# Kernel tuning notes

Hardware: AMD Instinct MI355X
Metric: run time of the kernel (lower is better)

Reference implementation:

```python
import jax, jax.numpy as jnp
import numpy as np

B, S, D, E = 4, 4096, 1024, 8

def setup_inputs() -> dict:
    key = jax.random.key(0)
    k1, k2, k3, k4, k5 = jax.random.split(key, 5)
    scale = 1.0 / np.sqrt(D)
    return {
        "x": jax.random.normal(k1, (B, S, D), dtype=jnp.float32),
        "Wg": jax.random.normal(k2, (D, D), dtype=jnp.float32) * scale,   # gate Linear(D, D)
        "bg": jnp.zeros((D,), dtype=jnp.float32),
        "We": jax.random.normal(k3, (E, D, D), dtype=jnp.float32) * scale,  # per-expert Linear(D, D)
        "be": jnp.zeros((E, D), dtype=jnp.float32),
    }

def reference(x, Wg, bg, We, be):
    # gating network: Linear + Softmax over last dim (size D, per the original module)
    probs = jax.nn.softmax(x @ Wg + bg, axis=-1)           # [B,S,D]
    idx = jnp.argmax(probs, axis=-1)                        # [B,S], values in [0, D)
    p = jnp.take_along_axis(probs, idx[..., None], axis=-1)[..., 0]  # top-1 gate prob
    e_idx = idx % We.shape[0]                               # map argmax to expert id
    # run every expert densely, then select routed expert per token (top-1 switch routing)
    h = jax.nn.relu(jnp.einsum('bsd,edf->besf', x, We) + be[None, :, None, :])  # [B,E,S,D]
    onehot = jax.nn.one_hot(e_idx, We.shape[0], dtype=x.dtype)                   # [B,S,E]
    out = jnp.einsum('besf,bse->bsf', h, onehot) * p[..., None]                  # [B,S,D]
    return out
```

## Files before the change

kernel.cpp:

```cpp
#include <hip/hip_runtime.h>
#include <stdint.h>
#include <stddef.h>

#define TOK    16384
#define DDIM   1024
#define NEXP   8
#define BMT    128
#define RB_MAX 136
#define MARGIN 2.5e-2f
#define AMBIG_CAP 4096
#define BK     64

typedef __bf16 bf16x8 __attribute__((ext_vector_type(8)));
typedef float  f32x4  __attribute__((ext_vector_type(4)));
typedef unsigned short u16x8 __attribute__((ext_vector_type(8)));

__device__ __forceinline__ unsigned short f2bf(float f) {
    unsigned int u = __float_as_uint(f);
    u += 0x7fff + ((u >> 16) & 1);
    return (unsigned short)(u >> 16);
}

__device__ __forceinline__ void gload_lds16(const void* g, void* l) {
    __builtin_amdgcn_global_load_lds(
        (const __attribute__((address_space(1))) unsigned int*)g,
        (__attribute__((address_space(3))) unsigned int*)l, 16, 0, 0);
}

__global__ __launch_bounds__(256) void cvt_x(
    const float* __restrict__ x, unsigned short* __restrict__ xbf)
{
    const size_t t = ((size_t)blockIdx.x * 256 + threadIdx.x) * 8;
    const float4 v0 = *(const float4*)(x + t);
    const float4 v1 = *(const float4*)(x + t + 4);
    const float vv[8] = {v0.x, v0.y, v0.z, v0.w, v1.x, v1.y, v1.z, v1.w};
    u16x8 hh;
#pragma unroll
    for (int j = 0; j < 8; j++) hh[j] = f2bf(vv[j]);
    *(u16x8*)(xbf + t) = hh;
}

__global__ __launch_bounds__(256) void transpose_mat(
    const float* __restrict__ src0, unsigned short* __restrict__ dst0)
{
    __shared__ float tile[32][33];
    const int e  = blockIdx.z;
    const int k0 = blockIdx.x * 32;
    const int n0 = blockIdx.y * 32;
    const int tx = threadIdx.x;
    const int ty = threadIdx.y;
    const float* src = src0 + (size_t)e * DDIM * DDIM;
    unsigned short* dst = dst0 + (size_t)e * DDIM * DDIM;
#pragma unroll
    for (int r = 0; r < 4; r++)
        tile[ty + r * 8][tx] = src[(size_t)(k0 + ty + r * 8) * DDIM + n0 + tx];
    __syncthreads();
#pragma unroll
    for (int r = 0; r < 4; r++)
        dst[(size_t)(n0 + ty + r * 8) * DDIM + k0 + tx] = f2bf(tile[tx][ty + r * 8]);
}

__global__ __launch_bounds__(256) void gating_mfma(
    const unsigned short* __restrict__ xbf,
    const unsigned short* __restrict__ WgT,
    const float* __restrict__ bg, float* __restrict__ logits)
{
    __shared__ unsigned short Asm[128 * BK];
    __shared__ unsigned short Bsm[128 * BK];
    const int rb = blockIdx.x;
    const int nb = blockIdx.y;
    const int tid  = threadIdx.x;
    const int lane = tid & 63;
    const int wave = tid >> 6;
    const int q    = lane >> 4;
    const int m16  = lane & 15;
    const int wrow = (wave & 1) * 64;
    const int wcol = (wave >> 1) * 64;

    const unsigned short* Ag = xbf + (size_t)rb * 128 * DDIM;
    const unsigned short* Bg = WgT + (size_t)nb * 128 * DDIM;

    const unsigned short* pa[4];
    const unsigned short* pb[4];
#pragma unroll
    for (int i = 0; i < 4; i++) {
        const int idx = tid + i * 256;
        const int r = idx >> 3;
        const int c = idx & 7;
        const int g = (c ^ (r & 7)) * 8;
        pa[i] = Ag + (size_t)r * DDIM + g;
        pb[i] = Bg + (size_t)r * DDIM + g;
    }

    f32x4 acc[4][4];
#pragma unroll
    for (int i = 0; i < 4; i++)
#pragma unroll
        for (int j = 0; j < 4; j++) acc[i][j] = (f32x4){0.f, 0.f, 0.f, 0.f};

    for (int k0 = 0; k0 < DDIM; k0 += BK) {
#pragma unroll
        for (int i = 0; i < 4; i++) {
            gload_lds16(pa[i] + k0, &Asm[(tid + i * 256) * 8]);
            gload_lds16(pb[i] + k0, &Bsm[(tid + i * 256) * 8]);
        }
        __syncthreads();
#pragma unroll
        for (int s = 0; s < 2; s++) {
            const int cs = (((s << 2) + q) ^ (m16 & 7)) << 3;
            bf16x8 af[4], bfr[4];
#pragma unroll
            for (int i = 0; i < 4; i++)
                af[i] = *(const bf16x8*)&Asm[(wrow + i * 16 + m16) * BK + cs];
#pragma unroll
            for (int j = 0; j < 4; j++)
                bfr[j] = *(const bf16x8*)&Bsm[(wcol + j * 16 + m16) * BK + cs];
#pragma unroll
            for (int i = 0; i < 4; i++)
#pragma unroll
                for (int j = 0; j < 4; j++)
                    acc[i][j] = __builtin_amdgcn_mfma_f32_16x16x32_bf16(
                        af[i], bfr[j], acc[i][j], 0, 0, 0);
        }
        __syncthreads();
    }

    float bgv[4];
#pragma unroll
    for (int j = 0; j < 4; j++) bgv[j] = bg[nb * 128 + wcol + j * 16 + m16];
#pragma unroll
    for (int i = 0; i < 4; i++)
#pragma unroll
        for (int r = 0; r < 4; r++) {
            const int row = rb * 128 + wrow + i * 16 + q * 4 + r;
#pragma unroll
            for (int j = 0; j < 4; j++) {
                const int col = nb * 128 + wcol + j * 16 + m16;
                logits[(size_t)row * DDIM + col] = acc[i][j][r] + bgv[j];
            }
        }
}

__global__ __launch_bounds__(256) void row_stats(
    const float* __restrict__ logits, float* __restrict__ pout,
    int* __restrict__ eout, float* __restrict__ rmax_a, float* __restrict__ s_a,
    int* __restrict__ ambig, int* __restrict__ n_ambig)
{
    const int row  = blockIdx.x * 4 + (threadIdx.x >> 6);
    const int lane = threadIdx.x & 63;
    const float* L = logits + (size_t)row * DDIM;
    float vals[16];
#pragma unroll
    for (int i = 0; i < 4; i++)
        *(float4*)&vals[i * 4] = *(const float4*)&L[lane * 16 + i * 4];
    float m = vals[0]; int mi = lane * 16;
#pragma unroll
    for (int i = 1; i < 16; i++)
        if (vals[i] > m) { m = vals[i]; mi = lane * 16 + i; }
    for (int off = 32; off > 0; off >>= 1) {
        float ov = __shfl_down(m, off, 64);
        int   oi = __shfl_down(mi, off, 64);
        if (ov > m || (ov == m && oi < mi)) { m = ov; mi = oi; }
    }
    m  = __shfl(m, 0, 64);
    mi = __shfl(mi, 0, 64);
    float s = 0.f;
    int   c = 0;
#pragma unroll
    for (int i = 0; i < 16; i++) {
        s += expf(vals[i] - m);
        if (vals[i] >= m - MARGIN) c++;
    }
    for (int off = 32; off > 0; off >>= 1) {
        s += __shfl_xor(s, off, 64);
        c += __shfl_xor(c, off, 64);
    }
    if (lane == 0) {
        pout[row] = 1.0f / s;
        eout[row] = mi & (NEXP - 1);
        rmax_a[row] = m;
        s_a[row] = s;
        if (c > 1) {
            int k = atomicAdd(n_ambig, 1);
            if (k < AMBIG_CAP) ambig[k] = row;
        }
    }
}

__global__ __launch_bounds__(64) void fixup(
    const float* __restrict__ logits, const float* __restrict__ x,
    const float* __restrict__ Wg, const float* __restrict__ bg,
    const float* __restrict__ rmax_a, const float* __restrict__ s_a,
    const int* __restrict__ ambig, const int* __restrict__ n_ambig,
    int* __restrict__ eout, float* __restrict__ pout)
{
    int n = *n_ambig; if (n > AMBIG_CAP) n = AMBIG_CAP;
    if ((int)blockIdx.x >= n) return;
    const int row  = ambig[blockIdx.x];
    const int lane = threadIdx.x;
    const float rmax = rmax_a[row];
    const float* L = logits + (size_t)row * DDIM;
    __shared__ int scnt;
    __shared__ int scol[32];
    if (lane == 0) scnt = 0;
    __syncthreads();
    for (int j = lane; j < DDIM; j += 64)
        if (L[j] >= rmax - MARGIN) {
            int k = atomicAdd(&scnt, 1);
            if (k < 32) scol[k] = j;
        }
    __syncthreads();
    int ncand = scnt < 32 ? scnt : 32;
    double bestv = -1e300; int bestc = DDIM;
    for (int cidx = 0; cidx < ncand; cidx++) {
        const int col = scol[cidx];
        double s = 0.0;
        for (int k = lane; k < DDIM; k += 64)
            s += (double)x[(size_t)row * DDIM + k] * (double)Wg[(size_t)k * DDIM + col];
        for (int off = 32; off > 0; off >>= 1) s += __shfl_down(s, off, 64);
        s = __shfl(s, 0, 64);
        s += (double)bg[col];
        if (s > bestv || (s == bestv && col < bestc)) { bestv = s; bestc = col; }
    }
    if (lane == 0) {
        eout[row] = bestc & (NEXP - 1);
        pout[row] = expf(L[bestc] - rmax) / s_a[row];
    }
}

__global__ __launch_bounds__(256) void histo(const int* __restrict__ eout,
                                             int* __restrict__ cnt)
{
    __shared__ int h[NEXP];
    if (threadIdx.x < NEXP) h[threadIdx.x] = 0;
    __syncthreads();
    const int t = blockIdx.x * 256 + threadIdx.x;
    if (t < TOK) atomicAdd(&h[eout[t]], 1);
    __syncthreads();
    if (threadIdx.x < NEXP) atomicAdd(&cnt[threadIdx.x], h[threadIdx.x]);
}

__global__ void compute_offsets(const int* __restrict__ cnt,
                                int* __restrict__ start,
                                int* __restrict__ blk_expert)
{
    if (threadIdx.x == 0 && blockIdx.x == 0) {
        int st[NEXP + 1];
        int total = 0;
        for (int e = 0; e < NEXP; e++) {
            st[e] = total;
            total += ((cnt[e] + BMT - 1) / BMT) * BMT;
        }
        st[NEXP] = total;
        for (int e = 0; e <= NEXP; e++) start[e] = st[e];
        for (int rb = 0; rb < RB_MAX; rb++) {
            int s = rb * BMT;
            int ex = -1;
            for (int e = 0; e < NEXP; e++)
                if (s >= st[e] && s < st[e + 1]) ex = e;
            blk_expert[rb] = ex;
        }
    }
}

__global__ __launch_bounds__(256) void assign_slots(
    const int* __restrict__ eout, const int* __restrict__ start,
    int* __restrict__ cursor, int* __restrict__ row_of_slot)
{
    __shared__ int h[NEXP];
    __shared__ int base[NEXP];
    const int tid = threadIdx.x;
    if (tid < NEXP) h[tid] = 0;
    __syncthreads();
    const int t = blockIdx.x * 256 + tid;
    int e = 0, lr = 0;
    if (t < TOK) {
        e = eout[t];
        lr = atomicAdd(&h[e], 1);
    }
    __syncthreads();
    if (tid < NEXP && h[tid] > 0)
        base[tid] = atomicAdd(&cursor[tid], h[tid]);
    __syncthreads();
    if (t < TOK)
        row_of_slot[start[e] + base[e] + lr] = t;
}

__global__ __launch_bounds__(256) void expert_gemm(
    const unsigned short* __restrict__ xbf, const unsigned short* __restrict__ WeT,
    const float* __restrict__ be, const float* __restrict__ p,
    const int* __restrict__ row_of_slot, const int* __restrict__ blk_expert,
    float* __restrict__ out)
{
    __shared__ unsigned short Asm[128 * BK];
    __shared__ unsigned short Bsm[128 * BK];
    __shared__ int rs[128];
    const int rb = blockIdx.x;
    const int nb = blockIdx.y;
    const int e = blk_expert[rb];
    if (e < 0) return;

    const int tid  = threadIdx.x;
    const int lane = tid & 63;
    const int wave = tid >> 6;
    const int q    = lane >> 4;
    const int m16  = lane & 15;
    const int wrow = (wave & 1) * 64;
    const int wcol = (wave >> 1) * 64;

    if (tid < 128) rs[tid] = row_of_slot[rb * 128 + tid];
    __syncthreads();

    const unsigned short* Bglob = WeT + (size_t)e * DDIM * DDIM + (size_t)nb * 128 * DDIM;

    const unsigned short* pa[4];
    const unsigned short* pb[4];
#pragma unroll
    for (int i = 0; i < 4; i++) {
        const int idx = tid + i * 256;
        const int r = idx >> 3;
        const int c = idx & 7;
        const int g = (c ^ (r & 7)) * 8;
        int tr = rs[r]; if (tr < 0) tr = 0;
        pa[i] = xbf + (size_t)tr * DDIM + g;
        pb[i] = Bglob + (size_t)r * DDIM + g;
    }

    f32x4 acc[4][4];
#pragma unroll
    for (int i = 0; i < 4; i++)
#pragma unroll
        for (int j = 0; j < 4; j++) acc[i][j] = (f32x4){0.f, 0.f, 0.f, 0.f};

    for (int k0 = 0; k0 < DDIM; k0 += BK) {
#pragma unroll
        for (int i = 0; i < 4; i++) {
            gload_lds16(pa[i] + k0, &Asm[(tid + i * 256) * 8]);
            gload_lds16(pb[i] + k0, &Bsm[(tid + i * 256) * 8]);
        }
        __syncthreads();
#pragma unroll
        for (int s = 0; s < 2; s++) {
            const int cs = (((s << 2) + q) ^ (m16 & 7)) << 3;
            bf16x8 af[4], bfr[4];
#pragma unroll
            for (int i = 0; i < 4; i++)
                af[i] = *(const bf16x8*)&Asm[(wrow + i * 16 + m16) * BK + cs];
#pragma unroll
            for (int j = 0; j < 4; j++)
                bfr[j] = *(const bf16x8*)&Bsm[(wcol + j * 16 + m16) * BK + cs];
#pragma unroll
            for (int i = 0; i < 4; i++)
#pragma unroll
                for (int j = 0; j < 4; j++)
                    acc[i][j] = __builtin_amdgcn_mfma_f32_16x16x32_bf16(
                        af[i], bfr[j], acc[i][j], 0, 0, 0);
        }
        __syncthreads();
    }

    float bev[4];
#pragma unroll
    for (int j = 0; j < 4; j++) bev[j] = be[e * DDIM + nb * 128 + wcol + j * 16 + m16];
#pragma unroll
    for (int i = 0; i < 4; i++)
#pragma unroll
        for (int r = 0; r < 4; r++) {
            const int t = rs[wrow + i * 16 + q * 4 + r];
            if (t < 0) continue;
            const float pv = p[t];
#pragma unroll
            for (int j = 0; j < 4; j++) {
                const int n = nb * 128 + wcol + j * 16 + m16;
                float v = acc[i][j][r] + bev[j];
                v = v > 0.f ? v : 0.f;
                out[(size_t)t * DDIM + n] = v * pv;
            }
        }
}

extern "C" void kernel_launch(void* const* d_in, const int* in_sizes, int n_in,
                              void* d_out, int out_size, void* d_ws, size_t ws_size,
                              hipStream_t stream)
{
    const float* x  = (const float*)d_in[0];
    const float* Wg = (const float*)d_in[1];
    const float* bg = (const float*)d_in[2];
    const float* We = (const float*)d_in[3];
    const float* be = (const float*)d_in[4];
    float* out = (float*)d_out;

    char* ws = (char*)d_ws;
    float* logits = (float*)ws;                 ws += (size_t)TOK * DDIM * 4;
    unsigned short* WeT = (unsigned short*)ws;  ws += (size_t)NEXP * DDIM * DDIM * 2;
    unsigned short* WgT = (unsigned short*)ws;  ws += (size_t)DDIM * DDIM * 2;
    unsigned short* xbf = (unsigned short*)ws;  ws += (size_t)TOK * DDIM * 2;
    float* p = (float*)ws;                      ws += (size_t)TOK * 4;
    int* e_arr = (int*)ws;                      ws += (size_t)TOK * 4;
    float* rmax_a = (float*)ws;                 ws += (size_t)TOK * 4;
    float* s_a = (float*)ws;                    ws += (size_t)TOK * 4;
    int* row_of_slot = (int*)ws;                ws += (size_t)RB_MAX * BMT * 4;
    int* cnt = (int*)ws;                        ws += NEXP * 4;
    int* cursor = (int*)ws;                     ws += NEXP * 4;
    int* start = (int*)ws;                      ws += (NEXP + 1) * 4;
    int* blk_expert = (int*)ws;                 ws += RB_MAX * 4;
    int* ambig = (int*)ws;                      ws += AMBIG_CAP * 4;
    int* n_ambig = (int*)ws;                    ws += 4;

    hipMemsetAsync(cnt, 0, NEXP * 4, stream);
    hipMemsetAsync(cursor, 0, NEXP * 4, stream);
    hipMemsetAsync(n_ambig, 0, 4, stream);
    hipMemsetAsync(row_of_slot, 0xFF, (size_t)RB_MAX * BMT * 4, stream);

    cvt_x<<<TOK * DDIM / (256 * 8), 256, 0, stream>>>(x, xbf);
    transpose_mat<<<dim3(32, 32, 1), dim3(32, 8), 0, stream>>>(Wg, WgT);
    transpose_mat<<<dim3(32, 32, NEXP), dim3(32, 8), 0, stream>>>(We, WeT);
    gating_mfma<<<dim3(TOK / 128, DDIM / 128), 256, 0, stream>>>(xbf, WgT, bg, logits);
    row_stats<<<TOK / 4, 256, 0, stream>>>(logits, p, e_arr, rmax_a, s_a, ambig, n_ambig);
    fixup<<<AMBIG_CAP, 64, 0, stream>>>(logits, x, Wg, bg, rmax_a, s_a, ambig, n_ambig, e_arr, p);
    histo<<<TOK / 256, 256, 0, stream>>>(e_arr, cnt);
    compute_offsets<<<1, 64, 0, stream>>>(cnt, start, blk_expert);
    assign_slots<<<TOK / 256, 256, 0, stream>>>(e_arr, start, cursor, row_of_slot);
    expert_gemm<<<dim3(RB_MAX, DDIM / 128), 256, 0, stream>>>(
        xbf, WeT, be, p, row_of_slot, blk_expert, out);
}
```

Before: 334.7 us.

## Double-buffer LDS tiles in gating and expert GEMMs to overlap loads

Both bf16 MFMA GEMM kernels now use two LDS buffers per operand. The next K-tile is issued via global_load_lds into the alternate buffer before computing on the current one, so global-load latency can hide behind MFMA work. This doubles LDS per block (from 32KB to 64KB), which may reduce occupancy. The loop keeps a trailing __syncthreads; correctness relies on the async LDS loads being waited on at that barrier.

Measured after the change: 355.7 us. 6.3% more time.

```diff
diff --git a/kernel.cpp b/kernel.cpp
--- a/kernel.cpp
+++ b/kernel.cpp
@@ -65,8 +65,8 @@
     const unsigned short* __restrict__ WgT,
     const float* __restrict__ bg, float* __restrict__ logits)
 {
-    __shared__ unsigned short Asm[128 * BK];
-    __shared__ unsigned short Bsm[128 * BK];
+    __shared__ unsigned short Asm[2][128 * BK];
+    __shared__ unsigned short Bsm[2][128 * BK];
     const int rb = blockIdx.x;
     const int nb = blockIdx.y;
     const int tid  = threadIdx.x;
@@ -98,23 +98,33 @@
 #pragma unroll
         for (int j = 0; j < 4; j++) acc[i][j] = (f32x4){0.f, 0.f, 0.f, 0.f};
 
-    for (int k0 = 0; k0 < DDIM; k0 += BK) {
-#pragma unroll
-        for (int i = 0; i < 4; i++) {
-            gload_lds16(pa[i] + k0, &Asm[(tid + i * 256) * 8]);
-            gload_lds16(pb[i] + k0, &Bsm[(tid + i * 256) * 8]);
-        }
-        __syncthreads();
+#pragma unroll
+    for (int i = 0; i < 4; i++) {
+        gload_lds16(pa[i], &Asm[0][(tid + i * 256) * 8]);
+        gload_lds16(pb[i], &Bsm[0][(tid + i * 256) * 8]);
+    }
+    __syncthreads();
+
+    int cur = 0;
+    for (int k0 = 0; k0 < DDIM; k0 += BK, cur ^= 1) {
+        const int nk = k0 + BK;
+        if (nk < DDIM) {
+#pragma unroll
+            for (int i = 0; i < 4; i++) {
+                gload_lds16(pa[i] + nk, &Asm[cur ^ 1][(tid + i * 256) * 8]);
+                gload_lds16(pb[i] + nk, &Bsm[cur ^ 1][(tid + i * 256) * 8]);
+            }
+        }
 #pragma unroll
         for (int s = 0; s < 2; s++) {
             const int cs = (((s << 2) + q) ^ (m16 & 7)) << 3;
             bf16x8 af[4], bfr[4];
 #pragma unroll
             for (int i = 0; i < 4; i++)
-                af[i] = *(const bf16x8*)&Asm[(wrow + i * 16 + m16) * BK + cs];
+                af[i] = *(const bf16x8*)&Asm[cur][(wrow + i * 16 + m16) * BK + cs];
 #pragma unroll
             for (int j = 0; j < 4; j++)
-                bfr[j] = *(const bf16x8*)&Bsm[(wcol + j * 16 + m16) * BK + cs];
+                bfr[j] = *(const bf16x8*)&Bsm[cur][(wcol + j * 16 + m16) * BK + cs];
 #pragma unroll
             for (int i = 0; i < 4; i++)
 #pragma unroll
@@ -292,8 +302,8 @@
     const int* __restrict__ row_of_slot, const int* __restrict__ blk_expert,
     float* __restrict__ out)
 {
-    __shared__ unsigned short Asm[128 * BK];
-    __shared__ unsigned short Bsm[128 * BK];
+    __shared__ unsigned short Asm[2][128 * BK];
+    __shared__ unsigned short Bsm[2][128 * BK];
     __shared__ int rs[128];
     const int rb = blockIdx.x;
     const int nb = blockIdx.y;
@@ -332,23 +342,33 @@
 #pragma unroll
         for (int j = 0; j < 4; j++) acc[i][j] = (f32x4){0.f, 0.f, 0.f, 0.f};
 
-    for (int k0 = 0; k0 < DDIM; k0 += BK) {
-#pragma unroll
-        for (int i = 0; i < 4; i++) {
-            gload_lds16(pa[i] + k0, &Asm[(tid + i * 256) * 8]);
-            gload_lds16(pb[i] + k0, &Bsm[(tid + i * 256) * 8]);
-        }
-        __syncthreads();
+#pragma unroll
+    for (int i = 0; i < 4; i++) {
+        gload_lds16(pa[i], &Asm[0][(tid + i * 256) * 8]);
+        gload_lds16(pb[i], &Bsm[0][(tid + i * 256) * 8]);
+    }
+    __syncthreads();
+
+    int cur = 0;
+    for (int k0 = 0; k0 < DDIM; k0 += BK, cur ^= 1) {
+        const int nk = k0 + BK;
+        if (nk < DDIM) {
+#pragma unroll
+            for (int i = 0; i < 4; i++) {
+                gload_lds16(pa[i] + nk, &Asm[cur ^ 1][(tid + i * 256) * 8]);
+                gload_lds16(pb[i] + nk, &Bsm[cur ^ 1][(tid + i * 256) * 8]);
+            }
+        }
 #pragma unroll
         for (int s = 0; s < 2; s++) {
             const int cs = (((s << 2) + q) ^ (m16 & 7)) << 3;
             bf16x8 af[4], bfr[4];
 #pragma unroll
             for (int i = 0; i < 4; i++)
-                af[i] = *(const bf16x8*)&Asm[(wrow + i * 16 + m16) * BK + cs];
+                af[i] = *(const bf16x8*)&Asm[cur][(wrow + i * 16 + m16) * BK + cs];
 #pragma unroll
             for (int j = 0; j < 4; j++)
-                bfr[j] = *(const bf16x8*)&Bsm[(wcol + j * 16 + m16) * BK + cs];
+                bfr[j] = *(const bf16x8*)&Bsm[cur][(wcol + j * 16 + m16) * BK + cs];
 #pragma unroll
             for (int i = 0; i < 4; i++)
 #pragma unroll
```
